# Kernel tuning notes

Hardware: AMD Instinct MI355X
Metric: run time of the kernel (lower is better)

Reference implementation:

```python
import jax, jax.numpy as jnp
import numpy as np

H = 16          # hidden_size
L = 24          # num_layers
LEN_TRAIN = 96
LEN_PRED = 48
B = 256         # leading dim of input (acts as TIME axis for the LSTMs, see notes)


def setup_inputs() -> dict:
    key = jax.random.key(0)
    ks = jax.random.split(key, 16)
    s = 1.0 / np.sqrt(H)  # PyTorch LSTM/Linear init scale
    u = lambda k, shp: jax.random.uniform(k, shp, jnp.float32, -s, s)
    return {
        "x": jax.random.normal(ks[0], (B, 1, LEN_TRAIN), jnp.float32),
        # lstm1: layer0 input_size=1, layers 1..23 input_size=2H
        "W_ih0_1": u(ks[1], (2, 4 * H, 1)),
        "W_ih_1": u(ks[2], (L - 1, 2, 4 * H, 2 * H)),
        "W_hh_1": u(ks[3], (L, 2, 4 * H, H)),
        "b_ih_1": u(ks[4], (L, 2, 4 * H)),
        "b_hh_1": u(ks[5], (L, 2, 4 * H)),
        # lstm2: all layers input_size=2H
        "W_ih_2": u(ks[6], (L, 2, 4 * H, 2 * H)),
        "W_hh_2": u(ks[7], (L, 2, 4 * H, H)),
        "b_ih_2": u(ks[8], (L, 2, 4 * H)),
        "b_hh_2": u(ks[9], (L, 2, 4 * H)),
        "fc1_w": u(ks[10], (1000, 2 * LEN_PRED * H)),
        "fc1_b": u(ks[11], (1000,)),
        "fc2_w": u(ks[12], (LEN_PRED, 1000)),
        "fc2_b": u(ks[13], (LEN_PRED,)),
    }


def _lstm_dir(x, Wih, Whh, bih, bhh, reverse):
    # x: (T, N, in). Precompute input-gate GEMM over whole sequence.
    xg = jnp.einsum("tni,gi->tng", x, Wih) + bih + bhh  # (T, N, 4H)

    def step(carry, g_in):
        h, c = carry
        g = g_in + h @ Whh.T
        i, f, gg, o = jnp.split(g, 4, axis=-1)  # PyTorch gate order i,f,g,o
        c = jax.nn.sigmoid(f) * c + jax.nn.sigmoid(i) * jnp.tanh(gg)
        h = jax.nn.sigmoid(o) * jnp.tanh(c)
        return (h, c), h

    N = x.shape[1]
    init = (jnp.zeros((N, H), x.dtype), jnp.zeros((N, H), x.dtype))
    _, hs = jax.lax.scan(step, init, xg, reverse=reverse)
    return hs  # (T, N, H), in original time order


def _bilstm_stack(x, Wih_per_layer, Whh, bih, bhh):
    for l in range(Whh.shape[0]):
        Wih = Wih_per_layer[l]
        fwd = _lstm_dir(x, Wih[0], Whh[l, 0], bih[l, 0], bhh[l, 0], False)
        bwd = _lstm_dir(x, Wih[1], Whh[l, 1], bih[l, 1], bhh[l, 1], True)
        x = jnp.concatenate([fwd, bwd], axis=-1)  # (T, N, 2H)
    return x


def reference(x, W_ih0_1, W_ih_1, W_hh_1, b_ih_1, b_hh_1,
              W_ih_2, W_hh_2, b_ih_2, b_hh_2,
              fc1_w, fc1_b, fc2_w, fc2_b):
    xp = jnp.transpose(x, (0, 2, 1))  # (B, 96, 1); dim0 is the LSTM time axis (batch_first=False quirk)
    wih1 = [W_ih0_1] + [W_ih_1[i] for i in range(L - 1)]
    h = _bilstm_stack(xp, wih1, W_hh_1, b_ih_1, b_hh_1)      # (B, 96, 2H)
    x1 = h[:, -LEN_PRED:, :]                                  # (B, 48, 2H)
    wih2 = [W_ih_2[i] for i in range(L)]
    h2 = _bilstm_stack(x1, wih2, W_hh_2, b_ih_2, b_hh_2)      # (B, 48, 2H)
    z = h2 + x1
    flat = z.reshape(z.shape[0], -1)                          # (B, 1536)
    y = jax.nn.relu(flat @ fc1_w.T + fc1_b) @ fc2_w.T + fc2_b # (B, 48)
    return jnp.transpose(y.reshape(y.shape[0], LEN_PRED, 1), (0, 2, 1))  # (B, 1, 48)
```

## Files before the change

### kernel.cpp

```cpp
#include <hip/hip_runtime.h>


template <int SEL>
__device__ __forceinline__ float quad_bcast(float v) {
  return __int_as_float(__builtin_amdgcn_update_dpp(
      0, __float_as_int(v), SEL * 0x55, 0xF, 0xF, true));
}

__global__ __launch_bounds__(256) void lstm_chain(
    const float* __restrict__ x, const float* __restrict__ W_ih0_1,
    const float* __restrict__ W_ih_1, const float* __restrict__ W_hh_1,
    const float* __restrict__ b_ih_1, const float* __restrict__ b_hh_1,
    const float* __restrict__ W_ih_2, const float* __restrict__ W_hh_2,
    const float* __restrict__ b_ih_2, const float* __restrict__ b_hh_2,
    float* __restrict__ x1g, float* __restrict__ h2g) {
  __shared__ float xgF[256 * 64];
  __shared__ float xgB[256 * 64];

  const int tid = threadIdx.x;
  const int lane = tid & 63;
  const int w = tid >> 6;
  const int n = blockIdx.x;
  const int nlay = (n < 48) ? 24 : 48;

  for (int L = 0; L < nlay; ++L) {
    const bool s2 = (L >= 24);
    const int l = s2 ? (L - 24) : L;
    const float* bih = s2 ? b_ih_2 : b_ih_1;
    const float* bhh = s2 ? b_hh_2 : b_hh_1;
    const float biasF = bih[l * 128 + lane] + bhh[l * 128 + lane];
    const float biasB = bih[l * 128 + 64 + lane] + bhh[l * 128 + 64 + lane];

    if (L == 0) {
      xgF[tid * 64 + 32] = x[(size_t)tid * 96 + n];
      const float w0F = W_ih0_1[lane];
      const float w0B = W_ih0_1[64 + lane];
      __syncthreads();
      for (int ti = 0; ti < 64; ++ti) {
        const int t = w * 64 + ti;
        const float xs = xgF[t * 64 + 32];
        xgF[t * 64 + lane] = fmaf(w0F, xs, biasF);
        xgB[t * 64 + lane] = fmaf(w0B, xs, biasB);
      }
    } else {
      const float* Wih = s2 ? (W_ih_2 + (size_t)l * 4096)
                            : (W_ih_1 + (size_t)(l - 1) * 4096);
      float wf[32], wb[32];
      {
        const float4* wpF = reinterpret_cast<const float4*>(Wih + (size_t)lane * 32);
        const float4* wpB =
            reinterpret_cast<const float4*>(Wih + (size_t)(64 + lane) * 32);
#pragma unroll
        for (int q = 0; q < 8; ++q) {
          const float4 a = wpF[q];
          wf[4 * q + 0] = a.x; wf[4 * q + 1] = a.y;
          wf[4 * q + 2] = a.z; wf[4 * q + 3] = a.w;
          const float4 b = wpB[q];
          wb[4 * q + 0] = b.x; wb[4 * q + 1] = b.y;
          wb[4 * q + 2] = b.z; wb[4 * q + 3] = b.w;
        }
      }
      for (int ti = 0; ti < 64; ++ti) {
        const int t = w * 64 + ti;
        const float4* hf4 = reinterpret_cast<const float4*>(&xgF[t * 64 + 32]);
        const float4* hb4 = reinterpret_cast<const float4*>(&xgB[t * 64 + 48]);
        float4 in[8];
#pragma unroll
        for (int q = 0; q < 4; ++q) in[q] = hf4[q];
#pragma unroll
        for (int q = 0; q < 4; ++q) in[4 + q] = hb4[q];
        float a0 = biasF, a1 = 0.f, a2 = 0.f, a3 = 0.f;
        float c0 = biasB, c1 = 0.f, c2 = 0.f, c3 = 0.f;
#pragma unroll
        for (int q = 0; q < 8; ++q) {
          const float4 v = in[q];
          a0 = fmaf(wf[4 * q + 0], v.x, a0);
          a1 = fmaf(wf[4 * q + 1], v.y, a1);
          a2 = fmaf(wf[4 * q + 2], v.z, a2);
          a3 = fmaf(wf[4 * q + 3], v.w, a3);
          c0 = fmaf(wb[4 * q + 0], v.x, c0);
          c1 = fmaf(wb[4 * q + 1], v.y, c1);
          c2 = fmaf(wb[4 * q + 2], v.z, c2);
          c3 = fmaf(wb[4 * q + 3], v.w, c3);
        }
        xgF[t * 64 + lane] = (a0 + a1) + (a2 + a3);
        xgB[t * 64 + lane] = (c0 + c1) + (c2 + c3);
      }
    }
    __syncthreads();

    if (w < 2) {
      float* xg = w ? xgB : xgF;
      const int d = w;
      const int jj = lane >> 2, g = lane & 3;
      const int r = g * 16 + jj;
      const int hcol = 32 + d * 16 + jj;
      const float* Whh =
          s2 ? (W_hh_2 + (size_t)l * 2048) : (W_hh_1 + (size_t)l * 2048);
      float whh[16];
#pragma unroll
      for (int k = 0; k < 16; ++k) whh[k] = Whh[((size_t)d * 64 + r) * 16 + k];
      const float s_ = (g == 2) ? 2.885390082f : -1.442695041f;
      const float m_ = (g == 2) ? -2.0f : 1.0f;
      const float b_ = (g == 2) ? 1.0f : 0.0f;
      float hs[16];
#pragma unroll
      for (int k = 0; k < 16; ++k) hs[k] = 0.f;
      float c = 0.f;
      const int dt = d ? -1 : 1;
      int t = d ? 255 : 0;
      float cur0 = xg[t * 64 + r];
      float cur1 = xg[(t + dt) * 64 + r];

#define LSTM_STEP(CUR, TT)                                                \
  {                                                                       \
    float a0 = (CUR), a1 = 0.f, a2 = 0.f, a3 = 0.f;                       \
    _Pragma("unroll") for (int k = 0; k < 16; k += 4) {                   \
      a0 = fmaf(whh[k + 0], hs[k + 0], a0);                               \
      a1 = fmaf(whh[k + 1], hs[k + 1], a1);                               \
      a2 = fmaf(whh[k + 2], hs[k + 2], a2);                               \
      a3 = fmaf(whh[k + 3], hs[k + 3], a3);                               \
    }                                                                     \
    const float gv = (a0 + a1) + (a2 + a3);                               \
    const float e = __builtin_amdgcn_exp2f(s_ * gv);                      \
    const float v = fmaf(m_, __builtin_amdgcn_rcpf(1.0f + e), b_);        \
    const float si = quad_bcast<0>(v);                                    \
    const float sf = quad_bcast<1>(v);                                    \
    const float tg = quad_bcast<2>(v);                                    \
    const float so = quad_bcast<3>(v);                                    \
    c = fmaf(sf, c, si * tg);                                             \
    const float e2 = __builtin_amdgcn_exp2f(2.885390082f * c);            \
    const float th = fmaf(-2.0f, __builtin_amdgcn_rcpf(1.0f + e2), 1.0f); \
    const float h = so * th;                                              \
    if (g == 0) xg[(TT)*64 + hcol] = h;                                   \
    const int hbb = __float_as_int(h);                                    \
    _Pragma("unroll") for (int k = 0; k < 16; ++k) hs[k] =                \
        __int_as_float(__builtin_amdgcn_readlane(hbb, 4 * k));            \
  }

      for (int tt = 0; tt < 256; tt += 2) {
        const float nx0 = xg[((t + 2 * dt) & 255) * 64 + r];
        LSTM_STEP(cur0, t)
        const float nx1 = xg[((t + 3 * dt) & 255) * 64 + r];
        LSTM_STEP(cur1, t + dt)
        cur0 = nx0;
        cur1 = nx1;
        t += 2 * dt;
      }
#undef LSTM_STEP
    }
    __syncthreads();

    if ((L == 23 && n >= 48) || L == 47) {
      float* dst = (L == 23) ? x1g : h2g;
#pragma unroll
      for (int p = 0; p < 8; ++p) {
        const int idx = p * 256 + tid;
        const int t = idx >> 3, q = idx & 7;
        const float4 v =
            (q < 4) ? *reinterpret_cast<const float4*>(&xgF[t * 64 + 32 + q * 4])
                    : *reinterpret_cast<const float4*>(
                          &xgB[t * 64 + 48 + (q - 4) * 4]);
        *reinterpret_cast<float4*>(dst + (size_t)t * 1536 + (n - 48) * 32 +
                                   q * 4) = v;
      }
      __syncthreads();
    }
  }
}

__global__ __launch_bounds__(256) void fc1_kernel(
    const float* __restrict__ h2,
    const float* __restrict__ x1,
    const float* __restrict__ w1, const float* __restrict__ b1,
    float* __restrict__ y1) {
  __shared__ float Zs[16][68];
  __shared__ float Ws[16][68];
  const int tid = threadIdx.x;
  const int m0 = blockIdx.x * 64;
  const int b0 = blockIdx.y * 64;
  const int rr = tid >> 2;
  const int c4 = (tid & 3) * 4;
  const int tx = tid & 15, ty = tid >> 4;

  float acc[4][4];
#pragma unroll
  for (int i = 0; i < 4; ++i)
#pragma unroll
    for (int jj = 0; jj < 4; ++jj) acc[i][jj] = 0.f;

  const bool wvalid = (m0 + rr) < 1000;
  const float* zr = h2 + (size_t)(b0 + rr) * 1536 + c4;
  const float* zr2 = x1 + (size_t)(b0 + rr) * 1536 + c4;
  const float* wr = w1 + (size_t)(m0 + rr) * 1536 + c4;

  float4 za = *reinterpret_cast<const float4*>(zr);
  float4 zb = *reinterpret_cast<const float4*>(zr2);
  float4 wv = wvalid ? *reinterpret_cast<const float4*>(wr)
                     : make_float4(0.f, 0.f, 0.f, 0.f);

  for (int k0 = 0; k0 < 1536; k0 += 16) {
    Zs[c4 + 0][rr] = za.x + zb.x;
    Zs[c4 + 1][rr] = za.y + zb.y;
    Zs[c4 + 2][rr] = za.z + zb.z;
    Zs[c4 + 3][rr] = za.w + zb.w;
    Ws[c4 + 0][rr] = wv.x;
    Ws[c4 + 1][rr] = wv.y;
    Ws[c4 + 2][rr] = wv.z;
    Ws[c4 + 3][rr] = wv.w;
    if (k0 + 16 < 1536) {
      za = *reinterpret_cast<const float4*>(zr + k0 + 16);
      zb = *reinterpret_cast<const float4*>(zr2 + k0 + 16);
      if (wvalid) wv = *reinterpret_cast<const float4*>(wr + k0 + 16);
    }
    __syncthreads();
#pragma unroll
    for (int kk = 0; kk < 16; ++kk) {
      const float4 av = *reinterpret_cast<const float4*>(&Zs[kk][ty * 4]);
      const float4 bv = *reinterpret_cast<const float4*>(&Ws[kk][tx * 4]);
      const float a_[4] = {av.x, av.y, av.z, av.w};
      const float b_[4] = {bv.x, bv.y, bv.z, bv.w};
#pragma unroll
      for (int i = 0; i < 4; ++i)
#pragma unroll
        for (int jj = 0; jj < 4; ++jj)
          acc[i][jj] = fmaf(a_[i], b_[jj], acc[i][jj]);
    }
    __syncthreads();
  }
#pragma unroll
  for (int i = 0; i < 4; ++i) {
    const int b = b0 + ty * 4 + i;
#pragma unroll
    for (int jj = 0; jj < 4; ++jj) {
      const int m = m0 + tx * 4 + jj;
      if (m < 1000) {
        const float vo = acc[i][jj] + b1[m];
        y1[(size_t)b * 1000 + m] = vo > 0.f ? vo : 0.f;
      }
    }
  }
}

__global__ __launch_bounds__(64) void fc2_kernel(
    const float* __restrict__ y1, const float* __restrict__ w2,
    const float* __restrict__ b2, float* __restrict__ out) {
  __shared__ float ys[1000];
  const int b = blockIdx.x;
  for (int k = threadIdx.x; k < 1000; k += 64) ys[k] = y1[(size_t)b * 1000 + k];
  __syncthreads();
  const int p = threadIdx.x;
  if (p < 48) {
    float a0 = b2[p], a1 = 0.f, a2 = 0.f, a3 = 0.f;
    const float* wr = w2 + (size_t)p * 1000;
    for (int k = 0; k < 1000; k += 4) {
      const float4 wv = *reinterpret_cast<const float4*>(wr + k);
      a0 = fmaf(ys[k + 0], wv.x, a0);
      a1 = fmaf(ys[k + 1], wv.y, a1);
      a2 = fmaf(ys[k + 2], wv.z, a2);
      a3 = fmaf(ys[k + 3], wv.w, a3);
    }
    out[(size_t)b * 48 + p] = (a0 + a1) + (a2 + a3);
  }
}

extern "C" void kernel_launch(void* const* d_in, const int* in_sizes, int n_in,
                              void* d_out, int out_size, void* d_ws,
                              size_t ws_size, hipStream_t stream) {
  const float* x = (const float*)d_in[0];
  const float* W_ih0_1 = (const float*)d_in[1];
  const float* W_ih_1 = (const float*)d_in[2];
  const float* W_hh_1 = (const float*)d_in[3];
  const float* b_ih_1 = (const float*)d_in[4];
  const float* b_hh_1 = (const float*)d_in[5];
  const float* W_ih_2 = (const float*)d_in[6];
  const float* W_hh_2 = (const float*)d_in[7];
  const float* b_ih_2 = (const float*)d_in[8];
  const float* b_hh_2 = (const float*)d_in[9];
  const float* fc1_w = (const float*)d_in[10];
  const float* fc1_b = (const float*)d_in[11];
  const float* fc2_w = (const float*)d_in[12];
  const float* fc2_b = (const float*)d_in[13];

  float* ws = (float*)d_ws;
  float* x1g = ws;
  float* h2g = ws + 393216;
  float* y1 = ws + 786432;

  lstm_chain<<<96, 256, 0, stream>>>(x, W_ih0_1, W_ih_1, W_hh_1, b_ih_1,
                                     b_hh_1, W_ih_2, W_hh_2, b_ih_2, b_hh_2,
                                     x1g, h2g);
  fc1_kernel<<<dim3(16, 4), 256, 0, stream>>>(h2g, x1g, fc1_w, fc1_b, y1);
  fc2_kernel<<<256, 64, 0, stream>>>(y1, fc2_w, fc2_b, (float*)d_out);
}
```

Before: 2.633 ms.

## Run forward and backward LSTM recurrences interleaved in a single wavefront

The forward and backward recurrences of each bidirectional layer now run interleaved in wave 0, where before they ran in waves 0 and 1 separately. The recurrent weights for both directions are loaded up front into wave 0's registers. Interleaving two independent dependency chains lets each direction's latency (readlane broadcasts, exp/rcp, DPP) be hidden behind the other's instructions, instead of two waves contending for the same SIMD. The cost is twice the instruction count on one wave and higher register pressure.

```diff
diff --git a/kernel.cpp b/kernel.cpp
--- a/kernel.cpp
+++ b/kernel.cpp
@@ -30,6 +30,19 @@
     const float* bhh = s2 ? b_hh_2 : b_hh_1;
     const float biasF = bih[l * 128 + lane] + bhh[l * 128 + lane];
     const float biasB = bih[l * 128 + 64 + lane] + bhh[l * 128 + 64 + lane];
+
+    const int jj = lane >> 2, g = lane & 3;
+    const int r = g * 16 + jj;
+    float whF[16], whB[16];
+    if (w == 0) {
+      const float* Whh =
+          s2 ? (W_hh_2 + (size_t)l * 2048) : (W_hh_1 + (size_t)l * 2048);
+#pragma unroll
+      for (int k = 0; k < 16; ++k) {
+        whF[k] = Whh[(size_t)r * 16 + k];
+        whB[k] = Whh[((size_t)64 + r) * 16 + k];
+      }
+    }
 
     if (L == 0) {
       xgF[tid * 64 + 32] = x[(size_t)tid * 96 + n];
@@ -47,7 +60,8 @@
                             : (W_ih_1 + (size_t)(l - 1) * 4096);
       float wf[32], wb[32];
       {
-        const float4* wpF = reinterpret_cast<const float4*>(Wih + (size_t)lane * 32);
+        const float4* wpF =
+            reinterpret_cast<const float4*>(Wih + (size_t)lane * 32);
         const float4* wpB =
             reinterpret_cast<const float4*>(Wih + (size_t)(64 + lane) * 32);
 #pragma unroll
@@ -89,37 +103,26 @@
     }
     __syncthreads();
 
-    if (w < 2) {
-      float* xg = w ? xgB : xgF;
-      const int d = w;
-      const int jj = lane >> 2, g = lane & 3;
-      const int r = g * 16 + jj;
-      const int hcol = 32 + d * 16 + jj;
-      const float* Whh =
-          s2 ? (W_hh_2 + (size_t)l * 2048) : (W_hh_1 + (size_t)l * 2048);
-      float whh[16];
-#pragma unroll
-      for (int k = 0; k < 16; ++k) whh[k] = Whh[((size_t)d * 64 + r) * 16 + k];
+    if (w == 0) {
       const float s_ = (g == 2) ? 2.885390082f : -1.442695041f;
       const float m_ = (g == 2) ? -2.0f : 1.0f;
       const float b_ = (g == 2) ? 1.0f : 0.0f;
-      float hs[16];
-#pragma unroll
-      for (int k = 0; k < 16; ++k) hs[k] = 0.f;
-      float c = 0.f;
-      const int dt = d ? -1 : 1;
-      int t = d ? 255 : 0;
-      float cur0 = xg[t * 64 + r];
-      float cur1 = xg[(t + dt) * 64 + r];
-
-#define LSTM_STEP(CUR, TT)                                                \
+      float hsF[16], hsB[16];
+#pragma unroll
+      for (int k = 0; k < 16; ++k) { hsF[k] = 0.f; hsB[k] = 0.f; }
+      float cF = 0.f, cB = 0.f;
+      int tF = 0, tB = 255;
+      float curF0 = xgF[0 * 64 + r], curF1 = xgF[1 * 64 + r];
+      float curB0 = xgB[255 * 64 + r], curB1 = xgB[254 * 64 + r];
+
+#define LSTM_STEP(SFX, XG, CUR, TT, HCOL)                                 \
   {                                                                       \
     float a0 = (CUR), a1 = 0.f, a2 = 0.f, a3 = 0.f;                       \
     _Pragma("unroll") for (int k = 0; k < 16; k += 4) {                   \
-      a0 = fmaf(whh[k + 0], hs[k + 0], a0);                               \
-      a1 = fmaf(whh[k + 1], hs[k + 1], a1);                               \
-      a2 = fmaf(whh[k + 2], hs[k + 2], a2);                               \
-      a3 = fmaf(whh[k + 3], hs[k + 3], a3);                               \
+      a0 = fmaf(wh##SFX[k + 0], hs##SFX[k + 0], a0);                      \
+      a1 = fmaf(wh##SFX[k + 1], hs##SFX[k + 1], a1);                      \
+      a2 = fmaf(wh##SFX[k + 2], hs##SFX[k + 2], a2);                      \
+      a3 = fmaf(wh##SFX[k + 3], hs##SFX[k + 3], a3);                      \
     }                                                                     \
     const float gv = (a0 + a1) + (a2 + a3);                               \
     const float e = __builtin_amdgcn_exp2f(s_ * gv);                      \
@@ -128,24 +131,28 @@
     const float sf = quad_bcast<1>(v);                                    \
     const float tg = quad_bcast<2>(v);                                    \
     const float so = quad_bcast<3>(v);                                    \
-    c = fmaf(sf, c, si * tg);                                             \
-    const float e2 = __builtin_amdgcn_exp2f(2.885390082f * c);            \
+    c##SFX = fmaf(sf, c##SFX, si * tg);                                   \
+    const float e2 = __builtin_amdgcn_exp2f(2.885390082f * c##SFX);       \
     const float th = fmaf(-2.0f, __builtin_amdgcn_rcpf(1.0f + e2), 1.0f); \
     const float h = so * th;                                              \
-    if (g == 0) xg[(TT)*64 + hcol] = h;                                   \
+    if (g == 0) XG[(TT)*64 + (HCOL)] = h;                                 \
     const int hbb = __float_as_int(h);                                    \
-    _Pragma("unroll") for (int k = 0; k < 16; ++k) hs[k] =                \
+    _Pragma("unroll") for (int k = 0; k < 16; ++k) hs##SFX[k] =           \
         __int_as_float(__builtin_amdgcn_readlane(hbb, 4 * k));            \
   }
 
       for (int tt = 0; tt < 256; tt += 2) {
-        const float nx0 = xg[((t + 2 * dt) & 255) * 64 + r];
-        LSTM_STEP(cur0, t)
-        const float nx1 = xg[((t + 3 * dt) & 255) * 64 + r];
-        LSTM_STEP(cur1, t + dt)
-        cur0 = nx0;
-        cur1 = nx1;
-        t += 2 * dt;
+        const float nxF0 = xgF[((tF + 2) & 255) * 64 + r];
+        const float nxB0 = xgB[((tB - 2) & 255) * 64 + r];
+        LSTM_STEP(F, xgF, curF0, tF, 32 + jj)
+        LSTM_STEP(B, xgB, curB0, tB, 48 + jj)
+        const float nxF1 = xgF[((tF + 3) & 255) * 64 + r];
+        const float nxB1 = xgB[((tB - 3) & 255) * 64 + r];
+        LSTM_STEP(F, xgF, curF1, tF + 1, 32 + jj)
+        LSTM_STEP(B, xgB, curB1, tB - 1, 48 + jj)
+        curF0 = nxF0; curB0 = nxB0;
+        curF1 = nxF1; curB1 = nxB1;
+        tF += 2; tB -= 2;
       }
 #undef LSTM_STEP
     }
```

Result: slower. 3.902 ms (+48.2%).
